# Performance work log

Hardware: AMD Instinct MI355X
Metric: run time of the kernel (lower is better)

## Reference

```python
import jax, jax.numpy as jnp
import numpy as np

GRID = (8192, 8192)   # 2D lattice, *dims
NDIM = 2              # links.shape[0]
P_LINK = 0.45         # subcritical bond probability -> finite clusters, bounded step count


def setup_inputs() -> dict:
    key = jax.random.key(0)
    k1, k2 = jax.random.split(key)
    # links[i] marks an open bond between site x and its +1 neighbour along axis i
    links = jax.random.uniform(k1, (NDIM,) + GRID) < P_LINK
    seed_idx = jax.random.randint(k2, (NDIM,), 0, GRID[0]).astype(jnp.int32)
    return {"links": links, "seed_idx": seed_idx}


def _flood_fill(links, seed_idx):
    """Faithful port of ClusterSelection.from_seed_idx: BFS-style roll+mask
    expansion iterated to fixed point via lax.while_loop."""
    ndim = links.shape[0]
    grid = links.shape[1:]
    selected0 = jnp.zeros(grid, dtype=bool).at[tuple(seed_idx)].set(True)

    def cond(carry):
        _, is_done, _ = carry
        return ~is_done

    def body(carry):
        sel0, _, steps = carry
        sel = sel0
        for i in range(ndim):  # unrolled over the (small, static) ndim
            # sites whose -1-neighbour or self is selected can use bond i
            links_to_try = sel0 | jnp.roll(sel0, -1, i)
            links_sel = links_to_try & links[i]
            # a taken bond marks both of its endpoints
            links_sel = links_sel | jnp.roll(links_sel, 1, i)
            sel = sel | links_sel
        is_done = (sel ^ sel0).sum() == 0
        return sel, is_done, steps + 1

    sel, _, steps = jax.lax.while_loop(
        cond, body, (selected0, jnp.array(False), jnp.array(0, jnp.int32))
    )
    return sel, steps


def reference(links, seed_idx):
    sel, _steps = _flood_fill(links, seed_idx)
    return sel
```

## Files before the change

### kernel.cpp

```cpp
#include <hip/hip_runtime.h>
#include <stdint.h>

#define GW 8192
#define GMASK 8191
#define PLANE 67108864ULL
#define TPD 128
#define TMASK 127
#define NTILES 16384
#define QCAP 16384
#define QMASK 16383
#define WPR 128

typedef unsigned long long u64;
typedef unsigned int u32;

__global__ void clear_bitmap_kernel(uint4* __restrict__ p, int n) {
    int i = blockIdx.x * blockDim.x + threadIdx.x;
    if (i < n) p[i] = make_uint4(0, 0, 0, 0);
}

__device__ __forceinline__ u32 nib4(u32 w) {
    return (((w & 0x01010101u) * 0x01020408u) >> 24) & 0xFu;
}
__device__ __forceinline__ u64 pack_row_b8(const unsigned char* p) {
    const uint4* q = (const uint4*)p;
    u64 w = 0;
#pragma unroll
    for (int i = 0; i < 4; i++) {
        uint4 v = q[i];
        u64 nb = (u64)(nib4(v.x) | (nib4(v.y) << 4) | (nib4(v.z) << 8) | (nib4(v.w) << 12));
        w |= nb << (16 * i);
    }
    return w;
}
__device__ __forceinline__ u64 pack_row_b32(const u32* p) {
    u64 w = 0;
#pragma unroll
    for (int k = 0; k < 16; k++) {
        uint4 v = ((const uint4*)p)[k];
        u64 nb = (u64)((v.x != 0) | ((v.y != 0) << 1) | ((v.z != 0) << 2) | ((v.w != 0) << 3));
        w |= nb << (4 * k);
    }
    return w;
}

__global__ void __launch_bounds__(1024)
bfs_tiles_kernel(const unsigned char* __restrict__ links8,
                 const int* __restrict__ seed_idx,
                 u64* __restrict__ bitmap) {
    volatile __shared__ unsigned short q[QCAP];
    __shared__ u32 tflags[NTILES / 32];
    __shared__ int s_qhead, s_qtail, s_active, s_mode, s_c1, s_c3;

    const int tid = threadIdx.x;
    const int ln  = tid & 63;

    for (int i = tid; i < QCAP; i += 1024) q[i] = 0xFFFF;
    for (int i = tid; i < NTILES / 32; i += 1024) tflags[i] = 0;
    if (tid == 0) { s_c1 = 0; s_c3 = 0; s_qhead = 0; s_qtail = 0; s_active = 0; }
    __syncthreads();

    int l1c = 0, l3c = 0;
    for (int i = tid; i < 16384; i += 1024) {
        if (links8[i]) { int m = i & 3; if (m == 1) l1c++; else if (m == 3) l3c++; }
    }
    atomicAdd(&s_c1, l1c);
    atomicAdd(&s_c3, l3c);
    __syncthreads();
    if (tid == 0) {
        s_mode = (s_c1 > 0) ? 0 : ((s_c3 > 0) ? 2 : 1);
        int sr = seed_idx[0] & GMASK, sc = seed_idx[1] & GMASK;
        atomicOr(&bitmap[(u64)sr * WPR + (sc >> 6)], 1ull << (sc & 63));
        int t = (sr >> 6) * TPD + (sc >> 6);
        tflags[t >> 5] = 1u << (t & 31);
        q[0] = (unsigned short)t;
        s_qtail = 1; s_active = 1;
    }
    __syncthreads();

    const int mode = s_mode;
    const unsigned char* p0b = links8;
    const unsigned char* p1b = links8 + PLANE;
    const u32* p0w = (const u32*)links8;
    const u32* p1w = (const u32*)(links8 + PLANE * 4);

    volatile int* v_head   = (volatile int*)&s_qhead;
    volatile int* v_tail   = (volatile int*)&s_qtail;
    volatile int* v_active = (volatile int*)&s_active;

    auto enq = [&](int t2) {
        u32 bit = 1u << (t2 & 31);
        u32 old = atomicOr(&tflags[t2 >> 5], bit);
        if (!(old & bit)) {
            atomicAdd(&s_active, 1);
            int pos = atomicAdd(&s_qtail, 1) & QMASK;
            q[pos] = (unsigned short)t2;
        }
    };

    long long guard = 0;
    while (true) {
        int t = -1;
        if (ln == 0) {
            while (true) {
                if (*v_active == 0) break;
                int h  = *v_head;
                int tl = *v_tail;
                if (h != tl) {
                    if (atomicCAS(&s_qhead, h, h + 1) == h) {
                        int pos = h & QMASK;
                        unsigned short v;
                        long long g2 = 0;
                        while ((v = q[pos]) == 0xFFFF) {
                            __builtin_amdgcn_s_sleep(1);
                            if (++g2 > 4000000LL) break;
                        }
                        q[pos] = 0xFFFF;
                        t = v;
                        break;
                    }
                } else {
                    __builtin_amdgcn_s_sleep(2);
                }
                if (++guard > 100000000LL) break;
            }
        }
        t = __shfl(t, 0);
        if (t < 0) break;

        const int tR = t >> 7, tC = t & TMASK;
        if (ln == 0) atomicAnd(&tflags[t >> 5], ~(1u << (t & 31)));
        __threadfence_block();

        const int gr = tR * 64 + ln;
        u64* wp = &bitmap[(u64)gr * WPR + tC];
        u64 loaded = *(volatile u64*)wp;

        u64 l0, l1;
        if (mode == 0) {
            l0 = pack_row_b8(p0b + (u64)gr * GW + tC * 64);
            l1 = pack_row_b8(p1b + (u64)gr * GW + tC * 64);
        } else {
            l0 = pack_row_b32(p0w + (u64)gr * GW + tC * 64);
            l1 = pack_row_b32(p1w + (u64)gr * GW + tC * 64);
        }

        u64 P0 = l1 & 0x7FFFFFFFFFFFFFFFull;
        u64 P1 = P0 & (P0 >> 1);
        u64 P2 = P1 & (P1 >> 2);
        u64 P3 = P2 & (P2 >> 4);
        u64 P4 = P3 & (P3 >> 8);
        u64 P5 = P4 & (P4 >> 16);
        u64 D0 = (ln < 63) ? l0 : 0ull;
        u64 D1 = D0 & __shfl_down(D0, 1);
        u64 D2 = D1 & __shfl_down(D1, 2);
        u64 D3 = D2 & __shfl_down(D2, 4);
        u64 D4 = D3 & __shfl_down(D3, 8);
        u64 D5 = D4 & __shfl_down(D4, 16);

        u64 sel = loaded;
        while (true) {
            u64 old = sel;
            sel |= (sel & P0) << 1;  sel |= (sel >> 1)  & P0;
            sel |= (sel & P1) << 2;  sel |= (sel >> 2)  & P1;
            sel |= (sel & P2) << 4;  sel |= (sel >> 4)  & P2;
            sel |= (sel & P3) << 8;  sel |= (sel >> 8)  & P3;
            sel |= (sel & P4) << 16; sel |= (sel >> 16) & P4;
            sel |= (sel & P5) << 32; sel |= (sel >> 32) & P5;
            sel |= __shfl_up(sel & D0, 1);  sel |= __shfl_down(sel, 1)  & D0;
            sel |= __shfl_up(sel & D1, 2);  sel |= __shfl_down(sel, 2)  & D1;
            sel |= __shfl_up(sel & D2, 4);  sel |= __shfl_down(sel, 4)  & D2;
            sel |= __shfl_up(sel & D3, 8);  sel |= __shfl_down(sel, 8)  & D3;
            sel |= __shfl_up(sel & D4, 16); sel |= __shfl_down(sel, 16) & D4;
            sel |= __shfl_up(sel & D5, 32); sel |= __shfl_down(sel, 32) & D5;
            if (__ballot(sel != old) == 0ull) break;
        }

        u64 newbits = sel & ~loaded;
        if (newbits) atomicOr(wp, newbits);

        const int c0 = tC * 64;
        bool rnew = false, lnew = false;
        if ((sel >> 63) & (l1 >> 63) & 1ull) {
            u64 old = atomicOr(&bitmap[(u64)gr * WPR + ((tC + 1) & TMASK)], 1ull);
            rnew = !(old & 1ull);
        }
        {
            u64 lcol = (u64)((c0 - 1) & GMASK);
            bool lopen = (mode == 0) ? (p1b[(u64)gr * GW + lcol] != 0)
                                     : (p1w[(u64)gr * GW + lcol] != 0);
            if ((sel & 1ull) && lopen) {
                u64 old = atomicOr(&bitmap[(u64)gr * WPR + ((tC - 1) & TMASK)], 1ull << 63);
                lnew = !(old & (1ull << 63));
            }
        }
        u64 rmask = __ballot(rnew), lmask = __ballot(lnew);

        const int ga = (tR * 64 - 1) & GMASK;
        bool bopen = (mode == 0) ? (p0b[(u64)ga * GW + c0 + ln] != 0)
                                 : (p0w[(u64)ga * GW + c0 + ln] != 0);
        u64 top_sel = __shfl(sel, 0);
        u64 umask = __ballot(bopen && ((top_sel >> ln) & 1));
        u64 unew = 0;
        if (ln == 0 && umask) {
            u64 old = atomicOr(&bitmap[(u64)ga * WPR + tC], umask);
            unew = umask & ~old;
        }
        u64 dmask = sel & l0;
        const int gb = (tR * 64 + 64) & GMASK;
        u64 dnew = 0;
        if (ln == 63 && dmask) {
            u64 old = atomicOr(&bitmap[(u64)gb * WPR + tC], dmask);
            dnew = dmask & ~old;
        }

        if (ln == 0  && rmask) enq(tR * TPD + ((tC + 1) & TMASK));
        if (ln == 1  && lmask) enq(tR * TPD + ((tC - 1) & TMASK));
        if (ln == 0  && unew)  enq(((tR - 1) & TMASK) * TPD + tC);
        if (ln == 63 && dnew)  enq(((tR + 1) & TMASK) * TPD + tC);

        if (ln == 0) atomicSub(&s_active, 1);
    }
}

__global__ void writeout_kernel(const u64* __restrict__ bitmap, int4* __restrict__ out) {
    int g = blockIdx.x * blockDim.x + threadIdx.x;
    int site0 = g << 2;
    u64 w = bitmap[site0 >> 6];
    u32 b = (u32)(w >> (site0 & 63)) & 0xFu;
    out[g] = make_int4(b & 1, (b >> 1) & 1, (b >> 2) & 1, (b >> 3) & 1);
}

extern "C" void kernel_launch(void* const* d_in, const int* in_sizes, int n_in,
                              void* d_out, int out_size, void* d_ws, size_t ws_size,
                              hipStream_t stream) {
    const unsigned char* links = (const unsigned char*)d_in[0];
    const int* seed = (const int*)d_in[1];

    u64* bitmap = (u64*)((char*)d_ws + 4096);

    clear_bitmap_kernel<<<2048, 256, 0, stream>>>((uint4*)bitmap, 524288);
    bfs_tiles_kernel<<<1, 1024, 0, stream>>>(links, seed, bitmap);
    writeout_kernel<<<65536, 256, 0, stream>>>(bitmap, (int4*)d_out);
}
```

Baseline: 662.6 us.

## Spread tile BFS work queue across 64 blocks using global-memory queue

Moves the tile work queue, tile flags and control counters from shared memory into the global workspace, and launches the BFS kernel with 64 blocks of 256 threads instead of a single 1024-thread block. The goal is to let more compute units process frontier tiles at once rather than being capped by one CU. Seeding and mode detection move into a separate init kernel, and the workspace clear grows to cover the new structures. The cost is agent-scope atomics and fences on every queue operation, which carry higher latency than shared-memory atomics and could limit throughput when the frontier is small.

```diff
diff --git a/kernel.cpp b/kernel.cpp
--- a/kernel.cpp
+++ b/kernel.cpp
@@ -7,16 +7,59 @@
 #define TPD 128
 #define TMASK 127
 #define NTILES 16384
-#define QCAP 16384
-#define QMASK 16383
+#define QCAP 65536
+#define QMASK 65535
 #define WPR 128
+
+#define OFF_CTRL   0
+#define OFF_TFLAGS 4096
+#define OFF_QUEUE  8192
+#define OFF_BITMAP 270336
+#define CLEAR_BYTES 8658944
 
 typedef unsigned long long u64;
 typedef unsigned int u32;
 
-__global__ void clear_bitmap_kernel(uint4* __restrict__ p, int n) {
+__device__ __forceinline__ u64 aload64(const u64* p) {
+    return __hip_atomic_load(p, __ATOMIC_RELAXED, __HIP_MEMORY_SCOPE_AGENT);
+}
+__device__ __forceinline__ int aload32(const int* p) {
+    return __hip_atomic_load(p, __ATOMIC_ACQUIRE, __HIP_MEMORY_SCOPE_AGENT);
+}
+
+__global__ void clear_ws_kernel(uint4* __restrict__ p, int n) {
     int i = blockIdx.x * blockDim.x + threadIdx.x;
     if (i < n) p[i] = make_uint4(0, 0, 0, 0);
+}
+
+__global__ void init_kernel(const unsigned char* __restrict__ links8,
+                            const int* __restrict__ seed_idx,
+                            char* __restrict__ ws) {
+    __shared__ int c1, c3;
+    if (threadIdx.x == 0) { c1 = 0; c3 = 0; }
+    __syncthreads();
+    int l1 = 0, l3 = 0;
+    for (int i = threadIdx.x; i < 16384; i += blockDim.x) {
+        if (links8[i]) { int m = i & 3; if (m == 1) l1++; else if (m == 3) l3++; }
+    }
+    atomicAdd(&c1, l1);
+    atomicAdd(&c3, l3);
+    __syncthreads();
+    if (threadIdx.x == 0) {
+        int* ctrl = (int*)(ws + OFF_CTRL);
+        u32* tflags = (u32*)(ws + OFF_TFLAGS);
+        int* q = (int*)(ws + OFF_QUEUE);
+        u64* bitmap = (u64*)(ws + OFF_BITMAP);
+        ctrl[3] = (c1 > 0) ? 0 : ((c3 > 0) ? 2 : 1);
+        int sr = seed_idx[0] & GMASK, sc = seed_idx[1] & GMASK;
+        bitmap[(u64)sr * WPR + (sc >> 6)] = 1ull << (sc & 63);
+        int t = (sr >> 6) * TPD + (sc >> 6);
+        tflags[t >> 5] = 1u << (t & 31);
+        q[0] = t + 1;
+        ctrl[0] = 0;
+        ctrl[1] = 1;
+        ctrl[2] = 1;
+    }
 }
 
 __device__ __forceinline__ u32 nib4(u32 w) {
@@ -44,57 +87,30 @@
     return w;
 }
 
-__global__ void __launch_bounds__(1024)
+__global__ void __launch_bounds__(256)
 bfs_tiles_kernel(const unsigned char* __restrict__ links8,
-                 const int* __restrict__ seed_idx,
-                 u64* __restrict__ bitmap) {
-    volatile __shared__ unsigned short q[QCAP];
-    __shared__ u32 tflags[NTILES / 32];
-    __shared__ int s_qhead, s_qtail, s_active, s_mode, s_c1, s_c3;
-
-    const int tid = threadIdx.x;
-    const int ln  = tid & 63;
-
-    for (int i = tid; i < QCAP; i += 1024) q[i] = 0xFFFF;
-    for (int i = tid; i < NTILES / 32; i += 1024) tflags[i] = 0;
-    if (tid == 0) { s_c1 = 0; s_c3 = 0; s_qhead = 0; s_qtail = 0; s_active = 0; }
-    __syncthreads();
-
-    int l1c = 0, l3c = 0;
-    for (int i = tid; i < 16384; i += 1024) {
-        if (links8[i]) { int m = i & 3; if (m == 1) l1c++; else if (m == 3) l3c++; }
-    }
-    atomicAdd(&s_c1, l1c);
-    atomicAdd(&s_c3, l3c);
-    __syncthreads();
-    if (tid == 0) {
-        s_mode = (s_c1 > 0) ? 0 : ((s_c3 > 0) ? 2 : 1);
-        int sr = seed_idx[0] & GMASK, sc = seed_idx[1] & GMASK;
-        atomicOr(&bitmap[(u64)sr * WPR + (sc >> 6)], 1ull << (sc & 63));
-        int t = (sr >> 6) * TPD + (sc >> 6);
-        tflags[t >> 5] = 1u << (t & 31);
-        q[0] = (unsigned short)t;
-        s_qtail = 1; s_active = 1;
-    }
-    __syncthreads();
-
-    const int mode = s_mode;
+                 char* __restrict__ ws) {
+    int* ctrl   = (int*)(ws + OFF_CTRL);
+    u32* tflags = (u32*)(ws + OFF_TFLAGS);
+    int* q      = (int*)(ws + OFF_QUEUE);
+    u64* bitmap = (u64*)(ws + OFF_BITMAP);
+
+    const int ln = threadIdx.x & 63;
+    const int mode = ctrl[3];
+
     const unsigned char* p0b = links8;
     const unsigned char* p1b = links8 + PLANE;
     const u32* p0w = (const u32*)links8;
     const u32* p1w = (const u32*)(links8 + PLANE * 4);
 
-    volatile int* v_head   = (volatile int*)&s_qhead;
-    volatile int* v_tail   = (volatile int*)&s_qtail;
-    volatile int* v_active = (volatile int*)&s_active;
-
     auto enq = [&](int t2) {
         u32 bit = 1u << (t2 & 31);
+        __threadfence();
         u32 old = atomicOr(&tflags[t2 >> 5], bit);
         if (!(old & bit)) {
-            atomicAdd(&s_active, 1);
-            int pos = atomicAdd(&s_qtail, 1) & QMASK;
-            q[pos] = (unsigned short)t2;
+            atomicAdd(&ctrl[2], 1);
+            int pos = atomicAdd(&ctrl[1], 1) & QMASK;
+            __hip_atomic_store(&q[pos], t2 + 1, __ATOMIC_RELEASE, __HIP_MEMORY_SCOPE_AGENT);
         }
     };
 
@@ -103,26 +119,28 @@
         int t = -1;
         if (ln == 0) {
             while (true) {
-                if (*v_active == 0) break;
-                int h  = *v_head;
-                int tl = *v_tail;
+                if (aload32(&ctrl[2]) == 0) break;
+                int h  = aload32(&ctrl[0]);
+                int tl = aload32(&ctrl[1]);
                 if (h != tl) {
-                    if (atomicCAS(&s_qhead, h, h + 1) == h) {
+                    if (atomicCAS((u32*)&ctrl[0], (u32)h, (u32)(h + 1)) == (u32)h) {
                         int pos = h & QMASK;
-                        unsigned short v;
+                        int v;
                         long long g2 = 0;
-                        while ((v = q[pos]) == 0xFFFF) {
+                        while ((v = __hip_atomic_load(&q[pos], __ATOMIC_ACQUIRE,
+                                                      __HIP_MEMORY_SCOPE_AGENT)) == 0) {
                             __builtin_amdgcn_s_sleep(1);
-                            if (++g2 > 4000000LL) break;
+                            if (++g2 > 10000000LL) break;
                         }
-                        q[pos] = 0xFFFF;
-                        t = v;
+                        __hip_atomic_store(&q[pos], 0, __ATOMIC_RELEASE,
+                                           __HIP_MEMORY_SCOPE_AGENT);
+                        t = v - 1;
                         break;
                     }
                 } else {
-                    __builtin_amdgcn_s_sleep(2);
+                    __builtin_amdgcn_s_sleep(8);
                 }
-                if (++guard > 100000000LL) break;
+                if (++guard > 200000000LL) break;
             }
         }
         t = __shfl(t, 0);
@@ -130,11 +148,11 @@
 
         const int tR = t >> 7, tC = t & TMASK;
         if (ln == 0) atomicAnd(&tflags[t >> 5], ~(1u << (t & 31)));
-        __threadfence_block();
+        __threadfence();
 
         const int gr = tR * 64 + ln;
         u64* wp = &bitmap[(u64)gr * WPR + tC];
-        u64 loaded = *(volatile u64*)wp;
+        u64 loaded = aload64(wp);
 
         u64 l0, l1;
         if (mode == 0) {
@@ -219,7 +237,8 @@
         if (ln == 0  && unew)  enq(((tR - 1) & TMASK) * TPD + tC);
         if (ln == 63 && dnew)  enq(((tR + 1) & TMASK) * TPD + tC);
 
-        if (ln == 0) atomicSub(&s_active, 1);
+        __threadfence();
+        if (ln == 0) atomicSub(&ctrl[2], 1);
     }
 }
 
@@ -236,10 +255,11 @@
                               hipStream_t stream) {
     const unsigned char* links = (const unsigned char*)d_in[0];
     const int* seed = (const int*)d_in[1];
-
-    u64* bitmap = (u64*)((char*)d_ws + 4096);
-
-    clear_bitmap_kernel<<<2048, 256, 0, stream>>>((uint4*)bitmap, 524288);
-    bfs_tiles_kernel<<<1, 1024, 0, stream>>>(links, seed, bitmap);
-    writeout_kernel<<<65536, 256, 0, stream>>>(bitmap, (int4*)d_out);
-}
+    char* ws = (char*)d_ws;
+
+    int n16 = CLEAR_BYTES / 16;
+    clear_ws_kernel<<<(n16 + 255) / 256, 256, 0, stream>>>((uint4*)ws, n16);
+    init_kernel<<<1, 256, 0, stream>>>(links, seed, ws);
+    bfs_tiles_kernel<<<64, 256, 0, stream>>>(links, ws);
+    writeout_kernel<<<65536, 256, 0, stream>>>((const u64*)(ws + OFF_BITMAP), (int4*)d_out);
+}
```

After: 705.3 us. +6.4%, slower.
